# Performance work log

Measured on AMD Instinct MI355X. Metric: run time of the kernel, lower is better.

## Reference

```python
import jax, jax.numpy as jnp
import numpy as np


def _tome_merge(xf, sim_w, dist_w):
    # xf: [B, t, C] tokens. Returns [B, t//2, C] merged tokens.
    t = xf.shape[1]
    h = t // 2
    width = int(t ** 0.5)
    metric = xf / jnp.linalg.norm(xf, axis=-1, keepdims=True)
    a_m, b_m = metric[:, :h, :], metric[:, h:, :]
    idx = jnp.arange(t)
    coords = jnp.stack([idx // width, idx % width], axis=-1).astype(jnp.float32)  # [t,2]
    ac, bc = coords[:h], coords[h:]
    sim = jnp.einsum('bic,bjc->bij', a_m, b_m)                      # [B,h,h]
    dist = jnp.sqrt(((ac[:, None, :] - bc[None, :, :]) ** 2).sum(-1))  # [h,h]
    scores = sim_w * sim + dist_w * (1.0 / (dist + 1e-6))
    dst = jnp.argmax(scores, axis=-1)                               # [B,h]
    a, b = xf[:, :h, :], xf[:, h:, :]

    def merge_one(a1, b1, d1):
        # scatter_reduce 'mean' with include_self=True: dst row counts itself
        s = b1.at[d1].add(a1)
        cnt = jnp.ones((h,), a1.dtype).at[d1].add(1.0)
        return s / cnt[:, None]

    return jax.vmap(merge_one)(a, b, dst)


def setup_inputs() -> dict:
    key = jax.random.key(0)
    k1, k2, k3, k4 = jax.random.split(key, 4)
    B, C, H, W = 8, 128, 64, 64
    out_ch = 128
    return {
        'x': jax.random.normal(k1, (B, C, H, W), dtype=jnp.float32),
        'sim_weight': jnp.float32(0.5),
        'dist_weight': jnp.float32(0.5),
        'conv_w': jax.random.normal(k2, (out_ch, C), dtype=jnp.float32) * 0.05,
        'bn_gamma': jax.random.uniform(k3, (out_ch,), dtype=jnp.float32, minval=0.5, maxval=1.5),
        'bn_beta': jax.random.normal(k4, (out_ch,), dtype=jnp.float32) * 0.1,
        'bn_mean': jnp.zeros((out_ch,), jnp.float32),
        'bn_var': jnp.ones((out_ch,), jnp.float32),
    }


def reference(x, sim_weight, dist_weight, conv_w, bn_gamma, bn_beta, bn_mean, bn_var):
    B, C, H, W = x.shape
    xf = x.reshape(B, C, H * W).transpose(0, 2, 1)        # [B, t, C]
    xf = _tome_merge(xf, sim_weight, dist_weight)          # t   -> t/2
    xf = _tome_merge(xf, sim_weight, dist_weight)          # t/2 -> t/4
    y = xf.transpose(0, 2, 1).reshape(B, C, H // 2, W // 2)
    # 1x1 conv + BatchNorm (eval) + SiLU
    y = jnp.einsum('bchw,oc->bohw', y, conv_w)
    eps = 1e-5
    scale = bn_gamma / jnp.sqrt(bn_var + eps)
    y = (y - bn_mean[None, :, None, None]) * scale[None, :, None, None] + bn_beta[None, :, None, None]
    return y * jax.nn.sigmoid(y)
```

## Files before the change

### kernel.cpp

```cpp
#include <hip/hip_runtime.h>
#include <math.h>

#define NB 8
#define NC 128

typedef _Float16 hf8 __attribute__((ext_vector_type(8)));
typedef _Float16 hf4 __attribute__((ext_vector_type(4)));
typedef float fx4 __attribute__((ext_vector_type(4)));

__global__ void lut_kernel(float* __restrict__ lut, const float* __restrict__ dwp,
                           int n) {
  int i = blockIdx.x * 256 + threadIdx.x;
  if (i < n) {
    float r = 1.0f / (sqrtf((float)i) + 1e-6f);
    lut[i] = dwp[0] * r;
  }
}

__global__ void prep_kernel(const float* __restrict__ x, float* __restrict__ xf,
                            float* __restrict__ nrm, _Float16* __restrict__ ext,
                            float* __restrict__ xf2, float* __restrict__ cnt1) {
  __shared__ float tile[64][129];
  __shared__ float part[64][4];
  __shared__ float rn_s[64];
  const int bid = blockIdx.x;
  const int b = bid & 7;
  const int p0 = (bid >> 3) * 64;
  const int tid = threadIdx.x;
  const int lane = tid & 63;
  const int q = tid >> 6;
  for (int cc = 0; cc < 32; ++cc) {
    int c = q * 32 + cc;
    tile[lane][c] = x[((size_t)(b * NC + c)) * 4096 + p0 + lane];
  }
  __syncthreads();
  float s = 0.f;
  for (int cc = 0; cc < 32; ++cc) {
    float v = tile[lane][q * 32 + cc];
    s += v * v;
  }
  part[lane][q] = s;
  __syncthreads();
  if (tid < 64) {
    float n = sqrtf(part[tid][0] + part[tid][1] + part[tid][2] + part[tid][3]);
    nrm[b * 4096 + p0 + tid] = n;
    rn_s[tid] = n;
  }
  __syncthreads();
  for (int it = 0; it < 8; ++it) {
    int idx = it * 256 + tid;
    int r = idx >> 5, e = (idx & 31) * 4;
    float4 v = make_float4(tile[r][e], tile[r][e + 1], tile[r][e + 2], tile[r][e + 3]);
    size_t o = (((size_t)b * 4096 + p0 + r) << 7) + e;
    *(float4*)&xf[o] = v;
    int tok = p0 + r;
    if (tok >= 2048) {
      size_t row2 = (size_t)b * 2048 + tok - 2048;
      *(float4*)&xf2[row2 * NC + e] = v;
      if (e == 0) cnt1[row2] = 1.0f;
    }
    if (ext != nullptr) {
      float n = rn_s[r];
      bool isA = tok < 2048;
      _Float16* rw = ext + ((size_t)b * 4096 + tok) * 256;
      float mm[4] = {v.x / n, v.y / n, v.z / n, v.w / n};
      hf4 hv, ov;
#pragma unroll
      for (int u = 0; u < 4; ++u) {
        float m = mm[u];
        _Float16 h = (_Float16)m;
        float hf_ = (float)h;
        hv[u] = h;
        ov[u] = isA ? (_Float16)((m - hf_) * 128.0f)
                    : (_Float16)(hf_ * 0.0078125f);
      }
      *(hf4*)&rw[e] = hv;
      *(hf4*)&rw[128 + e] = ov;
    }
  }
}

template <int WIDTH, int TT, int HH, int NJB>
__global__ __launch_bounds__(256, 4) void argmax_mfma6_kernel(
    const _Float16* __restrict__ ext, const float* __restrict__ swp,
    const float* __restrict__ dwp, unsigned long long* __restrict__ pu) {
  __shared__ _Float16 Bt[64][280];
  const int bid = blockIdx.x;
  const int b = bid & 7;
  const int rr = bid >> 3;
  const int jb = rr & (NJB - 1);
  const int ib = rr / NJB;
  const int tid = threadIdx.x;
  const int w = tid >> 6, l = tid & 63;
  const int lg = l >> 4, lm = l & 15;
  const int ipan = ib * 256 + w * 64;
  const int j0 = jb * 64;
  const float sw = swp[0], dwv = dwp[0];
  const _Float16* extb = ext + (size_t)b * TT * 256;
  const _Float16* brow0 = extb + (size_t)(HH + j0) * 256;

  const _Float16* ap[4];
#pragma unroll
  for (int s = 0; s < 4; ++s)
    ap[s] = extb + (size_t)(ipan + s * 16 + lm) * 256 + lg * 8;

  for (int f = tid; f < 64 * 32; f += 256) {
    int r = f >> 5, c = f & 31;
    *(float4*)&Bt[r][c * 8] = *(const float4*)&brow0[(size_t)r * 256 + c * 8];
  }
  __syncthreads();

  fx4 acc[4][4];
#pragma unroll
  for (int i4 = 0; i4 < 4; ++i4)
#pragma unroll
    for (int j4 = 0; j4 < 4; ++j4) acc[i4][j4] = 0.f;

#pragma unroll
  for (int kc = 0; kc < 8; ++kc) {
    hf8 af[4], bf[4];
#pragma unroll
    for (int s = 0; s < 4; ++s)
      af[s] = *(const hf8*)(ap[s] + kc * 32);
#pragma unroll
    for (int s = 0; s < 4; ++s)
      bf[s] = *(const hf8*)&Bt[s * 16 + lm][kc * 32 + lg * 8];
    __builtin_amdgcn_s_setprio(1);
#pragma unroll
    for (int j4 = 0; j4 < 4; ++j4)
#pragma unroll
      for (int i4 = 0; i4 < 4; ++i4)
        acc[i4][j4] = __builtin_amdgcn_mfma_f32_16x16x32_f16(
            af[i4], bf[j4], acc[i4][j4], 0, 0, 0);
    __builtin_amdgcn_s_setprio(0);
  }

  int jr4[4], jc4[4];
#pragma unroll
  for (int j4 = 0; j4 < 4; ++j4) {
    int tj = HH + j0 + j4 * 16 + lm;
    jr4[j4] = tj / WIDTH;
    jc4[j4] = tj % WIDTH;
  }
  __syncthreads();
  unsigned long long* rwv = (unsigned long long*)&Bt[0][0] + (size_t)w * 64 * 17;
#pragma unroll
  for (int i4 = 0; i4 < 4; ++i4) {
#pragma unroll
    for (int rg = 0; rg < 4; ++rg) {
      int il = i4 * 16 + lg * 4 + rg;
      int ti = ipan + il;
      int ir = ti / WIDTH, ic = ti % WIDTH;
      float bv = -1e30f;
      int bj = 0;
#pragma unroll
      for (int j4 = 0; j4 < 4; ++j4) {
        int dr = ir - jr4[j4], dc = ic - jc4[j4];
        float d2 = (float)(dr * dr + dc * dc);
        float sc = sw * acc[i4][j4][rg] + dwv * __builtin_amdgcn_rsqf(d2);
        int gj = j0 + j4 * 16 + lm;
        if (sc > bv) { bv = sc; bj = gj; }
      }
      rwv[il * 17 + lm] =
          ((unsigned long long)__float_as_uint(bv + 1.0f) << 32) |
          (unsigned)(~(unsigned)bj);
    }
  }
  __syncthreads();
  unsigned long long t1 = 0ull, t2 = 0ull;
#pragma unroll
  for (int c = 0; c < 16; ++c) {
    unsigned long long u = rwv[l * 17 + c];
    if (u > t1) { t2 = t1; t1 = u; }
    else if (u > t2) { t2 = u; }
  }
  size_t row = (size_t)b * HH + ipan + l;
  pu[row * (HH / 32) + jb * 2 + 0] = t1;
  pu[row * (HH / 32) + jb * 2 + 1] = t2;
}

template <int WIDTH, int TT, int HH, int NCH2>
__global__ __launch_bounds__(256) void tkrscat_kernel(
    const unsigned long long* __restrict__ pu, const float* __restrict__ xf,
    const float* __restrict__ nrm, const float* __restrict__ swp,
    const float* __restrict__ dwp, float* __restrict__ accbuf,
    float* __restrict__ cnt) {
  const int bid = blockIdx.x;
  const int bb = bid & 7;
  const int row = bb * HH + (bid >> 3) * 4 + (threadIdx.x >> 6);
  const int lane = threadIdx.x & 63;
  unsigned long long v = (lane < NCH2) ? pu[(size_t)row * NCH2 + lane] : 0ull;
  int candv[4];
#pragma unroll
  for (int t = 0; t < 4; ++t) {
    unsigned long long m = v;
#pragma unroll
    for (int off = 1; off < 64; off <<= 1) {
      unsigned long long o = __shfl_xor(m, off, 64);
      if (o > m) m = o;
    }
    candv[t] = (int)(~(unsigned)(m & 0xFFFFFFFFull));
    if (v == m) v = 0ull;
  }
  const int half = lane >> 5, ln = lane & 31;
  const int b = row / HH, i = row - b * HH;
  const float sw = swp[0], dwv = dwp[0];
  const float na = nrm[b * TT + i];
  float4 araw = *(const float4*)&xf[((size_t)b * TT + i) * NC + ln * 4];
  float4 a4 = make_float4(araw.x / na, araw.y / na, araw.z / na, araw.w / na);
  const int ir = i / WIDTH, ic = i % WIDTH;
  float bv = -3.0e38f;
  int bj = 0x7fffffff;
#pragma unroll
  for (int c = 0; c < 4; c += 2) {
    int j = candv[c + half];
    float4 b4 = *(const float4*)&xf[((size_t)b * TT + HH + j) * NC + ln * 4];
    float p = a4.x * b4.x + a4.y * b4.y + a4.z * b4.z + a4.w * b4.w;
#pragma unroll
    for (int off = 1; off < 32; off <<= 1) p += __shfl_xor(p, off, 32);
    float nb = nrm[b * TT + HH + j];
    int tj = HH + j;
    int jr = tj / WIDTH;
    int dr = ir - jr, dc = ic - (tj - jr * WIDTH);
    float r = 1.0f / (sqrtf((float)(dr * dr + dc * dc)) + 1e-6f);
    float sc = sw * (p / nb) + dwv * r;
    if (sc > bv || (sc == bv && j < bj)) { bv = sc; bj = j; }
  }
  {
    float ov = __shfl_xor(bv, 32, 64);
    int oj = __shfl_xor(bj, 32, 64);
    if (ov > bv || (ov == bv && oj < bj)) { bv = ov; bj = oj; }
  }
  if (half == 0) {
    float* base = &accbuf[((size_t)b * HH + bj) * NC + ln * 4];
    atomicAdd(base + 0, araw.x);
    atomicAdd(base + 1, araw.y);
    atomicAdd(base + 2, araw.z);
    atomicAdd(base + 3, araw.w);
    if (ln == 0) atomicAdd(&cnt[(size_t)b * HH + bj], 1.0f);
  }
}

template <int WIDTH, int TT, int HH, int IT, int JC>
__global__ __launch_bounds__(256, 4) void argmax2_kernel(
    const float* __restrict__ xf, const float* __restrict__ nrm,
    const float* __restrict__ swp, const float* __restrict__ lut,
    float* __restrict__ pval, int* __restrict__ pidx) {
  constexpr int MI = IT / 16;
  constexpr int NTILE = JC / 128;
  __shared__ float At[32][IT + 4];
  __shared__ float Bt[32][132];
  __shared__ int ico[2][IT];
  __shared__ int jco[2][JC];

  const int b = blockIdx.z;
  const int it0 = blockIdx.x * IT;
  const int jb = blockIdx.y;
  const int j0g = jb * JC;
  const int tid = threadIdx.x;

  for (int t = tid; t < IT; t += 256) {
    int tok = it0 + t;
    ico[0][t] = tok / WIDTH;
    ico[1][t] = tok % WIDTH;
  }
  for (int t = tid; t < JC; t += 256) {
    int tok = HH + j0g + t;
    jco[0][t] = tok / WIDTH;
    jco[1][t] = tok % WIDTH;
  }
  const float sw = swp[0];
  const float* srcb = xf + (size_t)b * TT * NC;

  const int ty = tid >> 4, tx = tid & 15;
  const int i0l = ty * MI;
  const int j0l = tx * 8;

  float best[MI];
  int bidx[MI];
#pragma unroll
  for (int ii = 0; ii < MI; ++ii) { best[ii] = -1e30f; bidx[ii] = 0; }

  for (int jt = 0; jt < NTILE; ++jt) {
    float acc[MI][8];
#pragma unroll
    for (int ii = 0; ii < MI; ++ii)
#pragma unroll
      for (int jj = 0; jj < 8; ++jj) acc[ii][jj] = 0.f;

    for (int kc = 0; kc < 4; ++kc) {
      __syncthreads();
#pragma unroll
      for (int p = 0; p < IT / 32; ++p) {
        int f = p * 256 + tid;
        int r = f >> 3, kq = (f & 7) * 4;
        const float* row = srcb + (size_t)(it0 + r) * NC + kc * 32 + kq;
        float4 v = *(const float4*)row;
        float n = nrm[b * TT + it0 + r];
        v.x /= n; v.y /= n; v.z /= n; v.w /= n;
        At[kq + 0][r] = v.x; At[kq + 1][r] = v.y;
        At[kq + 2][r] = v.z; At[kq + 3][r] = v.w;
      }
#pragma unroll
      for (int p = 0; p < 4; ++p) {
        int f = p * 256 + tid;
        int r = f >> 3, kq = (f & 7) * 4;
        int tok = HH + j0g + jt * 128 + r;
        const float* row = srcb + (size_t)tok * NC + kc * 32 + kq;
        float4 v = *(const float4*)row;
        float n = nrm[b * TT + tok];
        v.x /= n; v.y /= n; v.z /= n; v.w /= n;
        Bt[kq + 0][r] = v.x; Bt[kq + 1][r] = v.y;
        Bt[kq + 2][r] = v.z; Bt[kq + 3][r] = v.w;
      }
      __syncthreads();

#pragma unroll 4
      for (int k = 0; k < 32; ++k) {
        float a[MI], bb[8];
#pragma unroll
        for (int qv = 0; qv < MI / 4; ++qv)
          *(float4*)&a[qv * 4] = *(const float4*)&At[k][i0l + qv * 4];
        *(float4*)&bb[0] = *(const float4*)&Bt[k][j0l];
        *(float4*)&bb[4] = *(const float4*)&Bt[k][j0l + 4];
#pragma unroll
        for (int ii = 0; ii < MI; ++ii)
#pragma unroll
          for (int jj = 0; jj < 8; ++jj) acc[ii][jj] += a[ii] * bb[jj];
      }
    }

#pragma unroll
    for (int ii = 0; ii < MI; ++ii) {
      int ir = ico[0][i0l + ii], ic = ico[1][i0l + ii];
#pragma unroll
      for (int jj = 0; jj < 8; ++jj) {
        int jl = jt * 128 + j0l + jj;
        int dr = ir - jco[0][jl];
        int dc = ic - jco[1][jl];
        float sc = sw * acc[ii][jj] + lut[dr * dr + dc * dc];
        if (sc > best[ii]) {
          best[ii] = sc;
          bidx[ii] = j0g + jl;
        }
      }
    }
  }

  __syncthreads();
  float* rv = &At[0][0];
  int* rj = (int*)&Bt[0][0];
#pragma unroll
  for (int ii = 0; ii < MI; ++ii) {
    rv[(i0l + ii) * 17 + tx] = best[ii];
    rj[(i0l + ii) * 17 + tx] = bidx[ii];
  }
  __syncthreads();
  if (tid < IT) {
    float bv = rv[tid * 17];
    int bj = rj[tid * 17];
    for (int t = 1; t < 16; ++t) {
      float v = rv[tid * 17 + t];
      int j = rj[tid * 17 + t];
      if (v > bv || (v == bv && j < bj)) { bv = v; bj = j; }
    }
    int row = b * HH + it0 + tid;
    pval[(size_t)row * 8 + jb] = bv;
    pidx[(size_t)row * 8 + jb] = bj;
  }
}

__global__ void argreduce_kernel(const float* __restrict__ pv,
                                 const int* __restrict__ pj,
                                 int* __restrict__ dst, int nrows, int w) {
  int r = blockIdx.x * 256 + threadIdx.x;
  if (r >= nrows) return;
  const float* vv = pv + (size_t)r * w;
  const int* jj = pj + (size_t)r * w;
  float bv = vv[0];
  int bj = jj[0];
  for (int t = 1; t < w; ++t) {
    float v = vv[t];
    int j = jj[t];
    if (v > bv || (v == bv && j < bj)) { bv = v; bj = j; }
  }
  dst[r] = bj;
}

__global__ void scatter_kernel(const float* __restrict__ src,
                               const int* __restrict__ dst,
                               float* __restrict__ accbuf,
                               float* __restrict__ cnt, int HH, int TT) {
  const int b = blockIdx.x & 7;
  size_t local = (size_t)(blockIdx.x >> 3) * 256 + threadIdx.x;
  if (local >= (size_t)HH * 32) return;
  int i = (int)(local >> 5);
  int e = (int)(local & 31) * 4;
  float4 v = *(const float4*)&src[((size_t)b * TT + i) * NC + e];
  int d = dst[(size_t)b * HH + i];
  float* base = &accbuf[((size_t)b * HH + d) * NC + e];
  atomicAdd(base + 0, v.x);
  atomicAdd(base + 1, v.y);
  atomicAdd(base + 2, v.z);
  atomicAdd(base + 3, v.w);
  if (e == 0) atomicAdd(&cnt[(size_t)b * HH + d], 1.0f);
}

__global__ void finalize1_kernel(float* __restrict__ buf,
                                 const float* __restrict__ cnt,
                                 float* __restrict__ nrm,
                                 _Float16* __restrict__ ext,
                                 float* __restrict__ xf3,
                                 float* __restrict__ cnt2) {
  const int b = blockIdx.x & 7;
  int row = b * 2048 + (blockIdx.x >> 3) * 2 + (threadIdx.x >> 7);
  int c = threadIdx.x & 127;
  float v = buf[(size_t)row * NC + c] / cnt[row];
  buf[(size_t)row * NC + c] = v;
  int t = row & 2047;
  if (t >= 1024) {
    size_t r3 = (size_t)b * 1024 + t - 1024;
    xf3[r3 * NC + c] = v;
    if (c == 0) cnt2[r3] = 1.0f;
  }
  {
    float s = v * v;
    for (int off = 32; off > 0; off >>= 1) s += __shfl_down(s, off, 64);
    __shared__ float p[4];
    __shared__ float ns[2];
    int w = threadIdx.x >> 6;
    if ((threadIdx.x & 63) == 0) p[w] = s;
    __syncthreads();
    if ((threadIdx.x & 127) == 0) {
      float n = sqrtf(p[w] + p[w + 1]);
      nrm[row] = n;
      ns[threadIdx.x >> 7] = n;
    }
    __syncthreads();
    if (ext != nullptr) {
      float n = ns[threadIdx.x >> 7];
      float m = v / n;
      _Float16 h = (_Float16)m;
      float hf = (float)h;
      _Float16 ep = (_Float16)((m - hf) * 128.0f);
      _Float16 hs = (_Float16)(hf * 0.0078125f);
      bool isA = t < 1024;
      _Float16* rw = ext + (size_t)row * 256;
      rw[c] = h;
      rw[128 + c] = isA ? ep : hs;
    }
  }
}

__global__ __launch_bounds__(256) void conv_bn_silu_kernel(
    const float* __restrict__ xf3, const float* __restrict__ cnt2,
    const float* __restrict__ w, const float* __restrict__ gamma,
    const float* __restrict__ beta, const float* __restrict__ mean,
    const float* __restrict__ var, float* __restrict__ out) {
  __shared__ float X[64][132];
  __shared__ float Wt[128][68];
  const int b = blockIdx.x & 7, p0 = (blockIdx.x >> 3) * 64;
  const int tid = threadIdx.x, lane = tid & 63, q = tid >> 6;
  {
    const float cn = cnt2[(size_t)b * 1024 + p0 + lane];
    const float* row = xf3 + ((size_t)b * 1024 + p0 + lane) * NC;
    for (int cc = 0; cc < 8; ++cc) {
      int c = q * 32 + cc * 4;
      float4 v = *(const float4*)&row[c];
      X[lane][c + 0] = v.x / cn;
      X[lane][c + 1] = v.y / cn;
      X[lane][c + 2] = v.z / cn;
      X[lane][c + 3] = v.w / cn;
    }
  }
  const int ti = tid >> 4, tj = tid & 15;
  const int i4 = ti * 4, j4 = tj * 4;
  for (int ot = 0; ot < 2; ++ot) {
    __syncthreads();
    {
      const float* row = w + (size_t)(ot * 64 + lane) * NC;
      for (int cc = 0; cc < 8; ++cc) {
        int c = q * 32 + cc * 4;
        float4 v = *(const float4*)&row[c];
        Wt[c + 0][lane] = v.x;
        Wt[c + 1][lane] = v.y;
        Wt[c + 2][lane] = v.z;
        Wt[c + 3][lane] = v.w;
      }
    }
    __syncthreads();
    float acc[4][4];
#pragma unroll
    for (int ii = 0; ii < 4; ++ii)
#pragma unroll
      for (int jj = 0; jj < 4; ++jj) acc[ii][jj] = 0.f;

    for (int k = 0; k < NC; k += 4) {
      float4 a0 = *(const float4*)&X[i4 + 0][k];
      float4 a1 = *(const float4*)&X[i4 + 1][k];
      float4 a2 = *(const float4*)&X[i4 + 2][k];
      float4 a3 = *(const float4*)&X[i4 + 3][k];
      float4 b0 = *(const float4*)&Wt[k + 0][j4];
      float4 b1 = *(const float4*)&Wt[k + 1][j4];
      float4 b2 = *(const float4*)&Wt[k + 2][j4];
      float4 b3 = *(const float4*)&Wt[k + 3][j4];
#define FMA16(AX, BV)                                                     \
  acc[0][0] += a0.AX * BV.x; acc[0][1] += a0.AX * BV.y;                   \
  acc[0][2] += a0.AX * BV.z; acc[0][3] += a0.AX * BV.w;                   \
  acc[1][0] += a1.AX * BV.x; acc[1][1] += a1.AX * BV.y;                   \
  acc[1][2] += a1.AX * BV.z; acc[1][3] += a1.AX * BV.w;                   \
  acc[2][0] += a2.AX * BV.x; acc[2][1] += a2.AX * BV.y;                   \
  acc[2][2] += a2.AX * BV.z; acc[2][3] += a2.AX * BV.w;                   \
  acc[3][0] += a3.AX * BV.x; acc[3][1] += a3.AX * BV.y;                   \
  acc[3][2] += a3.AX * BV.z; acc[3][3] += a3.AX * BV.w;
      FMA16(x, b0)
      FMA16(y, b1)
      FMA16(z, b2)
      FMA16(w, b3)
#undef FMA16
    }

#pragma unroll
    for (int jj = 0; jj < 4; ++jj) {
      int o = ot * 64 + j4 + jj;
      float sc = gamma[o] / sqrtf(var[o] + 1e-5f);
      float mn = mean[o], bt = beta[o];
      float4 r;
      float z;
      z = (acc[0][jj] - mn) * sc + bt; r.x = z / (1.f + expf(-z));
      z = (acc[1][jj] - mn) * sc + bt; r.y = z / (1.f + expf(-z));
      z = (acc[2][jj] - mn) * sc + bt; r.z = z / (1.f + expf(-z));
      z = (acc[3][jj] - mn) * sc + bt; r.w = z / (1.f + expf(-z));
      *(float4*)&out[((size_t)(b * NC + o)) * 1024 + p0 + i4] = r;
    }
  }
}

extern "C" void kernel_launch(void* const* d_in, const int* in_sizes, int n_in,
                              void* d_out, int out_size, void* d_ws,
                              size_t ws_size, hipStream_t stream) {
  const float* x = (const float*)d_in[0];
  const float* swp = (const float*)d_in[1];
  const float* dwp = (const float*)d_in[2];
  const float* convw = (const float*)d_in[3];
  const float* gamma = (const float*)d_in[4];
  const float* beta = (const float*)d_in[5];
  const float* mean = (const float*)d_in[6];
  const float* var = (const float*)d_in[7];
  float* out = (float*)d_out;

  float* ws = (float*)d_ws;
  size_t o = 0;
  float* xf1 = ws + o;  o += (size_t)8 * 4096 * 128;
  float* nrm1 = ws + o; o += 8 * 4096;
  float* xf2 = ws + o;  o += (size_t)8 * 2048 * 128;
  float* nrm2 = ws + o; o += 8 * 2048;
  float* cnt1 = ws + o; o += 8 * 2048;
  float* cnt2 = ws + o; o += 8 * 1024;
  int* dst1 = (int*)(ws + o); o += 8 * 2048;
  int* dst2 = (int*)(ws + o); o += 8 * 1024;
  float* lut = ws + o;  o += 8192;
  unsigned long long* pu1 = (unsigned long long*)(ws + o);
  o += (size_t)8 * 2048 * 64 * 2;
  unsigned long long* pu2 = (unsigned long long*)(ws + o);
  o += (size_t)8 * 1024 * 32 * 2;
  _Float16* ext1 = (_Float16*)(ws + o);
  _Float16* ext2 = ext1;
  const size_t ext_floats = (size_t)8 * 4096 * 256 / 2;
  const bool mfma_ok = ws_size >= (o + ext_floats) * sizeof(float);
  float* xf3 = xf1;
  float* pv1 = (float*)pu1;
  int* pj1 = (int*)(pv1 + 8 * 2048 * 8);
  float* pv2 = (float*)pu2;
  int* pj2 = (int*)(pv2 + 8 * 1024 * 8);

  prep_kernel<<<512, 256, 0, stream>>>(x, xf1, nrm1, mfma_ok ? ext1 : nullptr,
                                       xf2, cnt1);
  if (mfma_ok) {
    argmax_mfma6_kernel<64, 4096, 2048, 32>
        <<<2048, 256, 0, stream>>>(ext1, swp, dwp, pu1);
    tkrscat_kernel<64, 4096, 2048, 64>
        <<<4096, 256, 0, stream>>>(pu1, xf1, nrm1, swp, dwp, xf2, cnt1);
  } else {
    lut_kernel<<<32, 256, 0, stream>>>(lut, dwp, 7939);
    argmax2_kernel<64, 4096, 2048, 128, 256>
        <<<dim3(16, 8, 8), 256, 0, stream>>>(xf1, nrm1, swp, lut, pv1, pj1);
    argreduce_kernel<<<64, 256, 0, stream>>>(pv1, pj1, dst1, 8 * 2048, 8);
    scatter_kernel<<<2048, 256, 0, stream>>>(xf1, dst1, xf2, cnt1, 2048, 4096);
  }
  finalize1_kernel<<<8192, 256, 0, stream>>>(xf2, cnt1, nrm2,
                                             mfma_ok ? ext2 : nullptr,
                                             xf3, cnt2);

  if (mfma_ok) {
    argmax_mfma6_kernel<45, 2048, 1024, 16>
        <<<512, 256, 0, stream>>>(ext2, swp, dwp, pu2);
    tkrscat_kernel<45, 2048, 1024, 32>
        <<<2048, 256, 0, stream>>>(pu2, xf2, nrm2, swp, dwp, xf3, cnt2);
  } else {
    argmax2_kernel<45, 2048, 1024, 64, 128>
        <<<dim3(16, 8, 8), 256, 0, stream>>>(xf2, nrm2, swp, lut, pv2, pj2);
    argreduce_kernel<<<32, 256, 0, stream>>>(pv2, pj2, dst2, 8 * 1024, 8);
    scatter_kernel<<<1024, 256, 0, stream>>>(xf2, dst2, xf3, cnt2, 1024, 2048);
  }

  conv_bn_silu_kernel<<<128, 256, 0, stream>>>(
      xf3, cnt2, convw, gamma, beta, mean, var, out);
}
```

Measured before the change: 153.8 us.

## Process two column tiles per block with swizzled LDS and shuffle-based top-2 reduction

The argmax kernel now walks two 64-column B tiles per block, so half as many blocks are launched and each A-fragment row set is reused across two tiles. The B tile in LDS is stored with an XOR swizzle instead of padding, and the MFMA operands are swapped so each lane holds a column group for a fixed row. The per-row top-2 reduction now runs in registers and finishes with cross-lane shuffles instead of going through an LDS scratch pass. In exchange there is an extra barrier per tile and fewer blocks to fill the GPU, and the A fragments are reloaded from global memory for the second tile.

Result: slower. 225.6 us (+46.6%).

```diff
diff --git a/kernel.cpp b/kernel.cpp
--- a/kernel.cpp
+++ b/kernel.cpp
@@ -80,103 +80,115 @@
   }
 }
 
-template <int WIDTH, int TT, int HH, int NJB>
-__global__ __launch_bounds__(256, 4) void argmax_mfma6_kernel(
+template <int WIDTH, int TT, int HH, int NJP>
+__global__ __launch_bounds__(256, 4) void argmax_mfma7_kernel(
     const _Float16* __restrict__ ext, const float* __restrict__ swp,
     const float* __restrict__ dwp, unsigned long long* __restrict__ pu) {
-  __shared__ _Float16 Bt[64][280];
+  __shared__ _Float16 Bt[64 * 256];
   const int bid = blockIdx.x;
   const int b = bid & 7;
   const int rr = bid >> 3;
-  const int jb = rr & (NJB - 1);
-  const int ib = rr / NJB;
+  const int jp = rr % NJP;
+  const int ib = rr / NJP;
   const int tid = threadIdx.x;
   const int w = tid >> 6, l = tid & 63;
   const int lg = l >> 4, lm = l & 15;
   const int ipan = ib * 256 + w * 64;
-  const int j0 = jb * 64;
   const float sw = swp[0], dwv = dwp[0];
   const _Float16* extb = ext + (size_t)b * TT * 256;
-  const _Float16* brow0 = extb + (size_t)(HH + j0) * 256;
 
   const _Float16* ap[4];
 #pragma unroll
   for (int s = 0; s < 4; ++s)
     ap[s] = extb + (size_t)(ipan + s * 16 + lm) * 256 + lg * 8;
 
-  for (int f = tid; f < 64 * 32; f += 256) {
-    int r = f >> 5, c = f & 31;
-    *(float4*)&Bt[r][c * 8] = *(const float4*)&brow0[(size_t)r * 256 + c * 8];
-  }
-  __syncthreads();
-
-  fx4 acc[4][4];
-#pragma unroll
-  for (int i4 = 0; i4 < 4; ++i4)
-#pragma unroll
-    for (int j4 = 0; j4 < 4; ++j4) acc[i4][j4] = 0.f;
-
-#pragma unroll
-  for (int kc = 0; kc < 8; ++kc) {
-    hf8 af[4], bf[4];
-#pragma unroll
-    for (int s = 0; s < 4; ++s)
-      af[s] = *(const hf8*)(ap[s] + kc * 32);
-#pragma unroll
-    for (int s = 0; s < 4; ++s)
-      bf[s] = *(const hf8*)&Bt[s * 16 + lm][kc * 32 + lg * 8];
-    __builtin_amdgcn_s_setprio(1);
-#pragma unroll
-    for (int j4 = 0; j4 < 4; ++j4)
-#pragma unroll
-      for (int i4 = 0; i4 < 4; ++i4)
-        acc[i4][j4] = __builtin_amdgcn_mfma_f32_16x16x32_f16(
-            af[i4], bf[j4], acc[i4][j4], 0, 0, 0);
-    __builtin_amdgcn_s_setprio(0);
-  }
-
-  int jr4[4], jc4[4];
-#pragma unroll
-  for (int j4 = 0; j4 < 4; ++j4) {
-    int tj = HH + j0 + j4 * 16 + lm;
-    jr4[j4] = tj / WIDTH;
-    jc4[j4] = tj % WIDTH;
-  }
-  __syncthreads();
-  unsigned long long* rwv = (unsigned long long*)&Bt[0][0] + (size_t)w * 64 * 17;
+  int ir4[4], ic4[4];
 #pragma unroll
   for (int i4 = 0; i4 < 4; ++i4) {
-#pragma unroll
-    for (int rg = 0; rg < 4; ++rg) {
-      int il = i4 * 16 + lg * 4 + rg;
-      int ti = ipan + il;
-      int ir = ti / WIDTH, ic = ti % WIDTH;
-      float bv = -1e30f;
-      int bj = 0;
+    int ti = ipan + i4 * 16 + lm;
+    ir4[i4] = ti / WIDTH;
+    ic4[i4] = ti % WIDTH;
+  }
+
+  for (int tt = 0; tt < 2; ++tt) {
+    const int jb = jp * 2 + tt;
+    const int j0 = jb * 64;
+    const _Float16* brow0 = extb + (size_t)(HH + j0) * 256;
+    if (tt) __syncthreads();
+    for (int f = tid; f < 64 * 32; f += 256) {
+      int r = f >> 5, u = f & 31;
+      int up = u ^ (r & 7);
+      *(float4*)&Bt[r * 256 + up * 8] =
+          *(const float4*)&brow0[(size_t)r * 256 + u * 8];
+    }
+    __syncthreads();
+
+    fx4 acc[4][4];
+#pragma unroll
+    for (int i4 = 0; i4 < 4; ++i4)
+#pragma unroll
+      for (int j4 = 0; j4 < 4; ++j4) acc[i4][j4] = 0.f;
+
+#pragma unroll
+    for (int kc = 0; kc < 8; ++kc) {
+      hf8 af[4], bf[4];
+#pragma unroll
+      for (int s = 0; s < 4; ++s)
+        af[s] = *(const hf8*)(ap[s] + kc * 32);
+#pragma unroll
+      for (int s = 0; s < 4; ++s) {
+        int up = (kc * 4 + lg) ^ (lm & 7);
+        bf[s] = *(const hf8*)&Bt[(s * 16 + lm) * 256 + up * 8];
+      }
+      __builtin_amdgcn_s_setprio(1);
+#pragma unroll
+      for (int j4 = 0; j4 < 4; ++j4)
+#pragma unroll
+        for (int i4 = 0; i4 < 4; ++i4)
+          acc[i4][j4] = __builtin_amdgcn_mfma_f32_16x16x32_f16(
+              bf[j4], af[i4], acc[i4][j4], 0, 0, 0);
+      __builtin_amdgcn_s_setprio(0);
+    }
+
+#pragma unroll
+    for (int i4 = 0; i4 < 4; ++i4) {
+      const int ir = ir4[i4], ic = ic4[i4];
+      unsigned long long t1 = 0ull, t2 = 0ull;
 #pragma unroll
       for (int j4 = 0; j4 < 4; ++j4) {
-        int dr = ir - jr4[j4], dc = ic - jc4[j4];
-        float d2 = (float)(dr * dr + dc * dc);
-        float sc = sw * acc[i4][j4][rg] + dwv * __builtin_amdgcn_rsqf(d2);
-        int gj = j0 + j4 * 16 + lm;
-        if (sc > bv) { bv = sc; bj = gj; }
-      }
-      rwv[il * 17 + lm] =
-          ((unsigned long long)__float_as_uint(bv + 1.0f) << 32) |
-          (unsigned)(~(unsigned)bj);
-    }
-  }
-  __syncthreads();
-  unsigned long long t1 = 0ull, t2 = 0ull;
-#pragma unroll
-  for (int c = 0; c < 16; ++c) {
-    unsigned long long u = rwv[l * 17 + c];
-    if (u > t1) { t2 = t1; t1 = u; }
-    else if (u > t2) { t2 = u; }
-  }
-  size_t row = (size_t)b * HH + ipan + l;
-  pu[row * (HH / 32) + jb * 2 + 0] = t1;
-  pu[row * (HH / 32) + jb * 2 + 1] = t2;
+#pragma unroll
+        for (int rg = 0; rg < 4; ++rg) {
+          int gj = j0 + j4 * 16 + lg * 4 + rg;
+          int tj = HH + gj;
+          int jr = tj / WIDTH, jc = tj % WIDTH;
+          int dr = ir - jr, dc = ic - jc;
+          float d2 = (float)(dr * dr + dc * dc);
+          float sc = sw * acc[i4][j4][rg] + dwv * __builtin_amdgcn_rsqf(d2);
+          unsigned long long u =
+              ((unsigned long long)__float_as_uint(sc + 1.0f) << 32) |
+              (unsigned)(~(unsigned)gj);
+          if (u > t1) { t2 = t1; t1 = u; }
+          else if (u > t2) { t2 = u; }
+        }
+      }
+#pragma unroll
+      for (int mk = 16; mk <= 32; mk <<= 1) {
+        unsigned long long o1 = __shfl_xor(t1, mk, 64);
+        unsigned long long o2 = __shfl_xor(t2, mk, 64);
+        if (o1 > t1) {
+          t2 = (t1 > o2) ? t1 : o2;
+          t1 = o1;
+        } else {
+          t2 = (t2 > o1) ? t2 : o1;
+        }
+      }
+      if (lg == 0) {
+        size_t row = (size_t)b * HH + ipan + i4 * 16 + lm;
+        pu[row * (HH / 32) + jb * 2 + 0] = t1;
+        pu[row * (HH / 32) + jb * 2 + 1] = t2;
+      }
+    }
+  }
 }
 
 template <int WIDTH, int TT, int HH, int NCH2>
@@ -577,8 +589,8 @@
   prep_kernel<<<512, 256, 0, stream>>>(x, xf1, nrm1, mfma_ok ? ext1 : nullptr,
                                        xf2, cnt1);
   if (mfma_ok) {
-    argmax_mfma6_kernel<64, 4096, 2048, 32>
-        <<<2048, 256, 0, stream>>>(ext1, swp, dwp, pu1);
+    argmax_mfma7_kernel<64, 4096, 2048, 16>
+        <<<1024, 256, 0, stream>>>(ext1, swp, dwp, pu1);
     tkrscat_kernel<64, 4096, 2048, 64>
         <<<4096, 256, 0, stream>>>(pu1, xf1, nrm1, swp, dwp, xf2, cnt1);
   } else {
@@ -593,8 +605,8 @@
                                              xf3, cnt2);
 
   if (mfma_ok) {
-    argmax_mfma6_kernel<45, 2048, 1024, 16>
-        <<<512, 256, 0, stream>>>(ext2, swp, dwp, pu2);
+    argmax_mfma7_kernel<45, 2048, 1024, 8>
+        <<<256, 256, 0, stream>>>(ext2, swp, dwp, pu2);
     tkrscat_kernel<45, 2048, 1024, 32>
         <<<2048, 256, 0, stream>>>(pu2, xf2, nrm2, swp, dwp, xf3, cnt2);
   } else {
```
